# Kernel optimization log

Measured on AMD Instinct MI355X. Metric: run time of the kernel, lower is better.

## Reference

```python
import jax, jax.numpy as jnp
import numpy as np

TEMPERATURE = 0.07
EPS = 1e-12  # matches torch F.normalize default eps


def setup_inputs() -> dict:
    key = jax.random.key(0)
    k1, k2 = jax.random.split(key)
    B, D = 8192, 256
    anchor = jax.random.normal(k1, (B, D), dtype=jnp.float32)
    positive = jax.random.normal(k2, (B, D), dtype=jnp.float32)
    return {"anchor": anchor, "positive": positive}


def _l2_normalize(x):
    # torch F.normalize(p=2, dim=1): x / max(||x||, eps)
    n = jnp.sqrt(jnp.sum(x * x, axis=1, keepdims=True))
    return x / jnp.maximum(n, EPS)


def reference(anchor, positive):
    a = _l2_normalize(anchor)
    p = _l2_normalize(positive)
    # normalized vectors -> cosine similarity is just a GEMM: (B, B)
    sim = jnp.einsum('id,jd->ij', a, p)
    B = sim.shape[0]
    # hard negative mining: max over off-diagonal entries per row
    neg = jnp.where(jnp.eye(B, dtype=bool), -jnp.inf, sim)
    max_neg = jnp.max(neg, axis=-1)  # (B,)
    logits = jnp.concatenate([sim, max_neg[:, None]], axis=1) / TEMPERATURE  # (B, B+1)
    labels = jnp.arange(B)
    logp = jax.nn.log_softmax(logits, axis=-1)
    loss = -jnp.mean(jnp.take_along_axis(logp, labels[:, None], axis=1))
    return loss
```

## Files before the change

kernel.cpp:

```cpp
#include <hip/hip_runtime.h>
#include <hip/hip_bf16.h>

using floatx4 = __attribute__((ext_vector_type(4))) float;
using int4v   = __attribute__((ext_vector_type(4))) int;
using int8v   = __attribute__((ext_vector_type(8))) int;

#define TEMP_INV 14.285714285714286f
#define DD 256
#define BM 128
#define NCT 4
#define SC1 127

typedef const __attribute__((address_space(1))) unsigned int* gptr_t;
typedef __attribute__((address_space(3))) unsigned int* lptr_t;

__device__ __forceinline__ void async_cp16(const void* g, void* l) {
  __builtin_amdgcn_global_load_lds((gptr_t)g, (lptr_t)l, 16, 0, 0);
}

__global__ __launch_bounds__(256) void nrm_kernel(
    const float* __restrict__ anchor, const float* __restrict__ positive,
    unsigned char* __restrict__ a8, unsigned char* __restrict__ p8,
    float* __restrict__ diag) {
  const int wave = threadIdx.x >> 6;
  const int lane = threadIdx.x & 63;
  const int row  = blockIdx.x * 4 + wave;
  const float4 va = ((const float4*)(anchor   + (size_t)row * DD))[lane];
  const float4 vp = ((const float4*)(positive + (size_t)row * DD))[lane];
  float sa = va.x * va.x + va.y * va.y + va.z * va.z + va.w * va.w;
  float sp = vp.x * vp.x + vp.y * vp.y + vp.z * vp.z + vp.w * vp.w;
#pragma unroll
  for (int m = 32; m >= 1; m >>= 1) {
    sa += __shfl_xor(sa, m, 64);
    sp += __shfl_xor(sp, m, 64);
  }
  const float ka = 1.0f / fmaxf(sqrtf(sa), 1e-12f);
  const float kp = 1.0f / fmaxf(sqrtf(sp), 1e-12f);
  int pa = __builtin_amdgcn_cvt_pk_fp8_f32(va.x * ka, va.y * ka, 0, false);
  pa     = __builtin_amdgcn_cvt_pk_fp8_f32(va.z * ka, va.w * ka, pa, true);
  int pp = __builtin_amdgcn_cvt_pk_fp8_f32(vp.x * kp, vp.y * kp, 0, false);
  pp     = __builtin_amdgcn_cvt_pk_fp8_f32(vp.z * kp, vp.w * kp, pp, true);
  ((int*)(a8 + (size_t)row * DD))[lane] = pa;
  ((int*)(p8 + (size_t)row * DD))[lane] = pp;
  float d = __builtin_amdgcn_cvt_f32_fp8(pa, 0) * __builtin_amdgcn_cvt_f32_fp8(pp, 0)
          + __builtin_amdgcn_cvt_f32_fp8(pa, 1) * __builtin_amdgcn_cvt_f32_fp8(pp, 1)
          + __builtin_amdgcn_cvt_f32_fp8(pa, 2) * __builtin_amdgcn_cvt_f32_fp8(pp, 2)
          + __builtin_amdgcn_cvt_f32_fp8(pa, 3) * __builtin_amdgcn_cvt_f32_fp8(pp, 3);
#pragma unroll
  for (int m = 32; m >= 1; m >>= 1) d += __shfl_xor(d, m, 64);
  if (lane == 0) diag[row] = d;
}

__device__ __forceinline__ int8v frag(const unsigned char* S, int row, int ks,
                                      int quad, int l16) {
  const int c0 = ks * 8 + quad * 2;
  const int4v lo = *(const int4v*)(S + row * DD + (((c0 + 0) ^ l16) << 4));
  const int4v hi = *(const int4v*)(S + row * DD + (((c0 + 1) ^ l16) << 4));
  return __builtin_shufflevector(lo, hi, 0, 1, 2, 3, 4, 5, 6, 7);
}

__global__ __launch_bounds__(512, 4) void gemm_stats(
    const unsigned char* __restrict__ a8, const unsigned char* __restrict__ p8,
    float* __restrict__ rsum, float* __restrict__ rmax, int Btot) {
  __shared__ __align__(16) unsigned char As[BM * DD];
  __shared__ __align__(16) unsigned char Bs[BM * DD];
  __shared__ float red_sum[2][BM];
  __shared__ float red_max[2][BM];

  const int t = threadIdx.x;
  const int wave = t >> 6, lane = t & 63;
  const int wm = wave & 3, wn = wave >> 2;
  const int quad = lane >> 4, l16 = lane & 15;
  const int row0    = blockIdx.y * BM;
  const int colbase = blockIdx.x * (NCT * BM);
  const bool hasdiag = ((int)(blockIdx.y >> 2) == (int)blockIdx.x);

  const int r4 = lane >> 4;
  const int cg = lane & 15;

#pragma unroll
  for (int q = 0; q < 4; ++q) {
    const int rb = q * 32 + wave * 4;
    const int r  = rb + r4;
    async_cp16(a8 + (size_t)(row0 + r) * DD + (cg ^ (r & 15)) * 16,
               &As[rb * DD]);
  }
#pragma unroll
  for (int q = 0; q < 4; ++q) {
    const int rb = q * 32 + wave * 4;
    const int r  = rb + r4;
    async_cp16(p8 + (size_t)(colbase + r) * DD + (cg ^ (r & 15)) * 16,
               &Bs[rb * DD]);
  }

  float se_run[2][4], mx_run[2][4];
#pragma unroll
  for (int a = 0; a < 2; ++a)
#pragma unroll
    for (int b = 0; b < 4; ++b) { se_run[a][b] = 0.f; mx_run[a][b] = -INFINITY; }

  for (int ct = 0; ct < NCT; ++ct) {
    __syncthreads();

    floatx4 acc[2][4];
#pragma unroll
    for (int a = 0; a < 2; ++a)
#pragma unroll
      for (int b = 0; b < 4; ++b) acc[a][b] = (floatx4){0.f, 0.f, 0.f, 0.f};

#pragma unroll
    for (int ks = 0; ks < 2; ++ks) {
      const int8v af0 = frag(As, wm * 32 + l16,      ks, quad, l16);
      const int8v af1 = frag(As, wm * 32 + 16 + l16, ks, quad, l16);
#pragma unroll
      for (int ni = 0; ni < 4; ++ni) {
        const int8v bf = frag(Bs, wn * 64 + ni * 16 + l16, ks, quad, l16);
        acc[0][ni] = __builtin_amdgcn_mfma_scale_f32_16x16x128_f8f6f4(
            af0, bf, acc[0][ni], 0, 0, 0, SC1, 0, SC1);
        acc[1][ni] = __builtin_amdgcn_mfma_scale_f32_16x16x128_f8f6f4(
            af1, bf, acc[1][ni], 0, 0, 0, SC1, 0, SC1);
      }
    }

    __syncthreads();
    if (ct + 1 < NCT) {
      const int colb = colbase + (ct + 1) * BM;
#pragma unroll
      for (int q = 0; q < 4; ++q) {
        const int rb = q * 32 + wave * 4;
        const int r  = rb + r4;
        async_cp16(p8 + (size_t)(colb + r) * DD + (cg ^ (r & 15)) * 16,
                   &Bs[rb * DD]);
      }
    }

    const int col0 = colbase + ct * BM;
    if (!hasdiag) {
#pragma unroll
      for (int mi = 0; mi < 2; ++mi)
#pragma unroll
        for (int reg = 0; reg < 4; ++reg)
#pragma unroll
          for (int ni = 0; ni < 4; ++ni) {
            const float s = acc[mi][ni][reg];
            se_run[mi][reg] += __expf(s * TEMP_INV);
            mx_run[mi][reg] = fmaxf(mx_run[mi][reg], s);
          }
    } else {
#pragma unroll
      for (int mi = 0; mi < 2; ++mi)
#pragma unroll
        for (int reg = 0; reg < 4; ++reg) {
          const int i = row0 + wm * 32 + mi * 16 + quad * 4 + reg;
#pragma unroll
          for (int ni = 0; ni < 4; ++ni) {
            const float s = acc[mi][ni][reg];
            const int j = col0 + wn * 64 + ni * 16 + l16;
            se_run[mi][reg] += __expf(s * TEMP_INV);
            mx_run[mi][reg] = fmaxf(mx_run[mi][reg], (i == j) ? -INFINITY : s);
          }
        }
    }
  }

#pragma unroll
  for (int mi = 0; mi < 2; ++mi) {
#pragma unroll
    for (int reg = 0; reg < 4; ++reg) {
      float se = se_run[mi][reg], mx = mx_run[mi][reg];
#pragma unroll
      for (int m = 1; m < 16; m <<= 1) {
        se += __shfl_xor(se, m, 64);
        mx = fmaxf(mx, __shfl_xor(mx, m, 64));
      }
      if (l16 == 0) {
        const int rb = wm * 32 + mi * 16 + quad * 4 + reg;
        red_sum[wn][rb] = se;
        red_max[wn][rb] = mx;
      }
    }
  }
  __syncthreads();
  if (t < BM) {
    rsum[(size_t)blockIdx.x * Btot + row0 + t] = red_sum[0][t] + red_sum[1][t];
    rmax[(size_t)blockIdx.x * Btot + row0 + t] = fmaxf(red_max[0][t], red_max[1][t]);
  }
}

__global__ __launch_bounds__(256) void row_loss_kernel(
    const float* __restrict__ rsum, const float* __restrict__ rmax,
    const float* __restrict__ diag, float* __restrict__ out, int Btot, int NG) {
  const int i = blockIdx.x * 256 + threadIdx.x;
  float s = 0.f, m = -INFINITY;
  for (int c = 0; c < NG; ++c) {
    s += rsum[(size_t)c * Btot + i];
    m = fmaxf(m, rmax[(size_t)c * Btot + i]);
  }
  float rl = __logf(s + __expf(m * TEMP_INV)) - diag[i] * TEMP_INV;
#pragma unroll
  for (int mm = 32; mm >= 1; mm >>= 1) rl += __shfl_xor(rl, mm, 64);
  __shared__ float red[4];
  if ((threadIdx.x & 63) == 0) red[threadIdx.x >> 6] = rl;
  __syncthreads();
  if (threadIdx.x == 0)
    atomicAdd(out, (red[0] + red[1] + red[2] + red[3]) / (float)Btot);
}

extern "C" void kernel_launch(void* const* d_in, const int* in_sizes, int n_in,
                              void* d_out, int out_size, void* d_ws, size_t ws_size,
                              hipStream_t stream) {
  const float* anchor   = (const float*)d_in[0];
  const float* positive = (const float*)d_in[1];
  const int B  = in_sizes[0] / DD;
  const int NG = B / (BM * NCT);
  const size_t BD = (size_t)B * DD;

  unsigned char* a8 = (unsigned char*)d_ws;
  unsigned char* p8 = a8 + BD;
  float* rsum  = (float*)(p8 + BD);
  float* rmax  = rsum + (size_t)NG * B;
  float* diag  = rmax + (size_t)NG * B;

  (void)hipMemsetAsync(d_out, 0, sizeof(float), stream);
  nrm_kernel<<<B / 4, 256, 0, stream>>>(anchor, positive, a8, p8, diag);
  dim3 g2(NG, B / BM);
  gemm_stats<<<g2, 512, 0, stream>>>(a8, p8, rsum, rmax, B);
  row_loss_kernel<<<B / 256, 256, 0, stream>>>(rsum, rmax, diag, (float*)d_out, B, NG);
}
```

Baseline: 102.3 us.

## Double-buffer B tiles through registers instead of direct global-to-LDS loads

Replaces the async global_load_lds copies with register-staged loads followed by swizzled LDS stores, and double-buffers the B tile in LDS. The next column tile is loaded into registers before the MFMA loop of the current tile, which removes the second barrier per iteration. This costs extra LDS (the B buffer grows from 32 KB to 64 KB), more registers, and the launch_bounds occupancy hint is dropped, so fewer blocks may fit per CU.

```diff
diff --git a/kernel.cpp b/kernel.cpp
--- a/kernel.cpp
+++ b/kernel.cpp
@@ -10,13 +10,6 @@
 #define BM 128
 #define NCT 4
 #define SC1 127
-
-typedef const __attribute__((address_space(1))) unsigned int* gptr_t;
-typedef __attribute__((address_space(3))) unsigned int* lptr_t;
-
-__device__ __forceinline__ void async_cp16(const void* g, void* l) {
-  __builtin_amdgcn_global_load_lds((gptr_t)g, (lptr_t)l, 16, 0, 0);
-}
 
 __global__ __launch_bounds__(256) void nrm_kernel(
     const float* __restrict__ anchor, const float* __restrict__ positive,
@@ -59,11 +52,25 @@
   return __builtin_shufflevector(lo, hi, 0, 1, 2, 3, 4, 5, 6, 7);
 }
 
-__global__ __launch_bounds__(512, 4) void gemm_stats(
+__device__ __forceinline__ void loadp(uint4* pr, const unsigned char* gbase, int t) {
+#pragma unroll
+  for (int k = 0; k < 4; ++k)
+    pr[k] = *(const uint4*)(gbase + (size_t)(k * 512 + t) * 16);
+}
+__device__ __forceinline__ void storep(unsigned char* lds, const uint4* pr, int t) {
+#pragma unroll
+  for (int k = 0; k < 4; ++k) {
+    const int c = k * 512 + t;
+    const int r = c >> 4, g = c & 15;
+    *(uint4*)(lds + r * DD + (((g ^ (r & 15))) << 4)) = pr[k];
+  }
+}
+
+__global__ __launch_bounds__(512) void gemm_stats(
     const unsigned char* __restrict__ a8, const unsigned char* __restrict__ p8,
     float* __restrict__ rsum, float* __restrict__ rmax, int Btot) {
   __shared__ __align__(16) unsigned char As[BM * DD];
-  __shared__ __align__(16) unsigned char Bs[BM * DD];
+  __shared__ __align__(16) unsigned char Bs[2][BM * DD];
   __shared__ float red_sum[2][BM];
   __shared__ float red_max[2][BM];
 
@@ -75,23 +82,11 @@
   const int colbase = blockIdx.x * (NCT * BM);
   const bool hasdiag = ((int)(blockIdx.y >> 2) == (int)blockIdx.x);
 
-  const int r4 = lane >> 4;
-  const int cg = lane & 15;
-
-#pragma unroll
-  for (int q = 0; q < 4; ++q) {
-    const int rb = q * 32 + wave * 4;
-    const int r  = rb + r4;
-    async_cp16(a8 + (size_t)(row0 + r) * DD + (cg ^ (r & 15)) * 16,
-               &As[rb * DD]);
-  }
-#pragma unroll
-  for (int q = 0; q < 4; ++q) {
-    const int rb = q * 32 + wave * 4;
-    const int r  = rb + r4;
-    async_cp16(p8 + (size_t)(colbase + r) * DD + (cg ^ (r & 15)) * 16,
-               &Bs[rb * DD]);
-  }
+  uint4 pr[4];
+  loadp(pr, a8 + (size_t)row0 * DD, t);
+  storep(As, pr, t);
+  loadp(pr, p8 + (size_t)colbase * DD, t);
+  __syncthreads();
 
   float se_run[2][4], mx_run[2][4];
 #pragma unroll
@@ -100,8 +95,11 @@
     for (int b = 0; b < 4; ++b) { se_run[a][b] = 0.f; mx_run[a][b] = -INFINITY; }
 
   for (int ct = 0; ct < NCT; ++ct) {
+    storep((unsigned char*)Bs[ct & 1], pr, t);
     __syncthreads();
-
+    if (ct + 1 < NCT)
+      loadp(pr, p8 + (size_t)(colbase + (ct + 1) * BM) * DD, t);
+    const unsigned char* Bh = Bs[ct & 1];
     floatx4 acc[2][4];
 #pragma unroll
     for (int a = 0; a < 2; ++a)
@@ -114,23 +112,11 @@
       const int8v af1 = frag(As, wm * 32 + 16 + l16, ks, quad, l16);
 #pragma unroll
       for (int ni = 0; ni < 4; ++ni) {
-        const int8v bf = frag(Bs, wn * 64 + ni * 16 + l16, ks, quad, l16);
+        const int8v bf = frag(Bh, wn * 64 + ni * 16 + l16, ks, quad, l16);
         acc[0][ni] = __builtin_amdgcn_mfma_scale_f32_16x16x128_f8f6f4(
             af0, bf, acc[0][ni], 0, 0, 0, SC1, 0, SC1);
         acc[1][ni] = __builtin_amdgcn_mfma_scale_f32_16x16x128_f8f6f4(
             af1, bf, acc[1][ni], 0, 0, 0, SC1, 0, SC1);
-      }
-    }
-
-    __syncthreads();
-    if (ct + 1 < NCT) {
-      const int colb = colbase + (ct + 1) * BM;
-#pragma unroll
-      for (int q = 0; q < 4; ++q) {
-        const int rb = q * 32 + wave * 4;
-        const int r  = rb + r4;
-        async_cp16(p8 + (size_t)(colb + r) * DD + (cg ^ (r & 15)) * 16,
-                   &Bs[rb * DD]);
       }
     }
 
```

New measurement: 125.4 us. 22.6% more time.
